# Optimization experiments

Hardware: AMD Instinct MI355X
Metric: run time of the kernel (lower is better)

Reference implementation:

```python
import jax, jax.numpy as jnp
import numpy as np

N_NODES = 4194304  # 2**22
LEVELS = 10
COARSE = 8192
RANK = 2
NNZ = 8388608


def _interp_linear(u, N):
    """torch F.interpolate(mode='linear', align_corners=False) along axis 1. u: (B,M,R) -> (B,N,R)."""
    M = u.shape[1]
    pos = (jnp.arange(N, dtype=jnp.float32) + 0.5) * (M / N) - 0.5
    pos = jnp.clip(pos, 0.0, M - 1)
    i0 = jnp.floor(pos).astype(jnp.int32)
    i1 = jnp.minimum(i0 + 1, M - 1)
    w = (pos - i0.astype(jnp.float32))[None, :, None]
    return u[:, i0] * (1.0 - w) + u[:, i1] * w


def _apply_hodlr(diag, u_factors, v_factors, x):
    B, N, _ = x.shape
    y = diag * x
    L = u_factors.shape[0]
    for lvl in range(L):
        num_splits = 2 ** (lvl + 1)
        bs = N // num_splits
        if bs == 0:
            continue
        uc, vc = u_factors[lvl], v_factors[lvl]
        u_full = _interp_linear(uc, N) if uc.shape[1] != N else uc
        v_full = _interp_linear(vc, N) if vc.shape[1] != N else vc
        P = num_splits // 2
        valid = P * 2 * bs
        xv = x[:, :valid].reshape(B, P, 2, bs, 1)
        uv = u_full[:, :valid].reshape(B, P, 2, bs, -1)
        vv = v_full[:, :valid].reshape(B, P, 2, bs, -1)
        xL, xR = xv[:, :, 0], xv[:, :, 1]
        uL, uR = uv[:, :, 0], uv[:, :, 1]
        vL, vR = vv[:, :, 0], vv[:, :, 1]
        xRp = jnp.einsum('bpkr,bpko->bpro', vR, xR)  # (B,P,R,1)
        xLp = jnp.einsum('bpkr,bpko->bpro', vL, xL)
        yL = jnp.einsum('bpkr,bpro->bpko', uL, xRp)  # (B,P,bs,1)
        yR = jnp.einsum('bpkr,bpro->bpko', uR, xLp)
        upd = jnp.stack([yL, yR], axis=2).reshape(B, valid, 1)
        if valid < N:
            upd = jnp.pad(upd, ((0, 0), (0, N - valid), (0, 0)))
        y = y + upd
    return y


def setup_inputs() -> dict:
    key = jax.random.key(0)
    ks = jax.random.split(key, 6)
    diag = jax.random.uniform(ks[0], (1, N_NODES, 1), dtype=jnp.float32)
    u_factors = jax.random.normal(ks[1], (LEVELS, 1, COARSE, RANK), dtype=jnp.float32)
    v_factors = jax.random.normal(ks[2], (LEVELS, 1, COARSE, RANK), dtype=jnp.float32)
    A_values = jax.random.normal(ks[3], (NNZ,), dtype=jnp.float32)
    z = jax.random.normal(ks[4], (1, N_NODES, 1), dtype=jnp.float32)
    A_indices = jax.random.randint(ks[5], (2, NNZ), 0, N_NODES, dtype=jnp.int64) if jax.config.jax_enable_x64 else jax.random.randint(ks[5], (2, NNZ), 0, N_NODES, dtype=jnp.int32)
    return {"diag": diag, "u_factors": u_factors, "v_factors": v_factors,
            "A_values": A_values, "z": z, "A_indices": A_indices, "num_nodes": N_NODES}


def reference(diag, u_factors, v_factors, A_values, z, A_indices, num_nodes):
    N = num_nodes
    w = _apply_hodlr(diag, u_factors, v_factors, z)          # (1,N,1)
    w_flat = w.reshape(N)
    rows, cols = A_indices[0], A_indices[1]
    y_flat = jax.ops.segment_sum(A_values * w_flat[cols], rows, num_segments=N)
    y = y_flat.reshape(1, N, 1)
    loss = jnp.mean((y - z) ** 2)
    return loss
```

## Files before the change

kernel.cpp:

```cpp
#include <hip/hip_runtime.h>

#define N_NODES 4194304
#define LEVELS  10
#define COARSE  8192
#define NNZ_E   8388608
#define NCHUNK  16384
#define NB      256
#define CB_SZ   16384
#define RB_SZ   16384
#define HB      1024
#define EPB     8192
#define TILE    8192

typedef int          v4i __attribute__((ext_vector_type(4)));
typedef float        v4f __attribute__((ext_vector_type(4)));
typedef unsigned int v4u __attribute__((ext_vector_type(4)));
typedef unsigned int v2u __attribute__((ext_vector_type(2)));

static __device__ __forceinline__ unsigned short f2bf(float x) {
    unsigned u = __float_as_uint(x);
    return (unsigned short)((u + 0x7FFFu + ((u >> 16) & 1u)) >> 16);
}
static __device__ __forceinline__ float bf2f(unsigned short h) {
    return __uint_as_float((unsigned)h << 16);
}
static __device__ __forceinline__ unsigned f18(float p) {
    return ((__float_as_uint(p) + 0x2000u) >> 14) & 0x3FFFFu;
}

__global__ __launch_bounds__(512) void kA(const float* __restrict__ z,
                                          float2* __restrict__ M,
                                          float* __restrict__ S,
                                          float* __restrict__ out,
                                          const int* __restrict__ rows,
                                          const int* __restrict__ cols,
                                          unsigned* __restrict__ colBO,
                                          unsigned* __restrict__ rowBC) {
    int b = blockIdx.x, t = threadIdx.x;
    if (b < 2048) {
        if (b == 0) {
            for (int i = t; i < 2046 * 2; i += 512) S[i] = 0.f;
            if (t == 0) out[0] = 0.f;
        }
        int lane = t & 63, wave = t >> 6;
        int chunk = b * 8 + wave;
        int base = chunk * 256 + lane * 4;
        float4 zv = *(const float4*)(z + base);
        float a0 = 0.f, a1 = 0.f;
        const float* zp = (const float*)&zv;
#pragma unroll
        for (int j = 0; j < 4; ++j) {
            float p = ((float)(base + j) + 0.5f) * (1.0f / 512.0f) - 0.5f;
            p = fminf(fmaxf(p, 0.0f), (float)(COARSE - 1));
            float f = p - floorf(p);
            a0 += zp[j] * (1.0f - f);
            a1 += zp[j] * f;
        }
#pragma unroll
        for (int off = 32; off >= 1; off >>= 1) {
            a0 += __shfl_xor(a0, off, 64);
            a1 += __shfl_xor(a1, off, 64);
        }
        if (lane == 0) M[chunk] = make_float2(a0, a1);
    } else {
        __shared__ unsigned hc[NB], hr[NB];
        int blk = b - 2048;
        if (t < 256) { hc[t] = 0u; hr[t] = 0u; }
        __syncthreads();
        int base = blk * EPB;
#pragma unroll
        for (int it = 0; it < 4; ++it) {
            int e = base + it * 2048 + t * 4;
            v4i r = __builtin_nontemporal_load((const v4i*)(rows + e));
            v4i c = __builtin_nontemporal_load((const v4i*)(cols + e));
            atomicAdd(&hr[r.x >> 14], 1u); atomicAdd(&hr[r.y >> 14], 1u);
            atomicAdd(&hr[r.z >> 14], 1u); atomicAdd(&hr[r.w >> 14], 1u);
            atomicAdd(&hc[c.x >> 14], 1u); atomicAdd(&hc[c.y >> 14], 1u);
            atomicAdd(&hc[c.z >> 14], 1u); atomicAdd(&hc[c.w >> 14], 1u);
        }
        __syncthreads();
        if (t < 256) {
            colBO[t * HB + blk] = hc[t];
            rowBC[t * HB + blk] = hr[t];
        }
    }
}

__global__ __launch_bounds__(256) void kB(const float2* __restrict__ M,
                                          const float* __restrict__ V,
                                          float* __restrict__ S,
                                          unsigned* __restrict__ colBO,
                                          unsigned* __restrict__ colTotal,
                                          const unsigned* __restrict__ rowBC,
                                          unsigned* __restrict__ rowTotal) {
    int b = blockIdx.x, t = threadIdx.x;
    if (b < 80) {
        int lvl = b >> 3, slice = b & 7;
        const float2* Vl = (const float2*)(V + lvl * COARSE * 2);
        float s0 = 0.f, s1 = 0.f;
        int c0 = slice * 2048 + t * 8;
#pragma unroll
        for (int cc = 0; cc < 8; ++cc) {
            int c = c0 + cc;
            float2 m = M[c];
            int k = (c > 0) ? ((c - 1) >> 1) : 0;
            int kp = min(k + 1, COARSE - 1);
            float2 vk = Vl[k], vkp = Vl[kp];
            s0 += vk.x * m.x + vkp.x * m.y;
            s1 += vk.y * m.x + vkp.y * m.y;
        }
        int gw = min(1 << (10 - lvl), 64);
        for (int sh = gw >> 1; sh >= 1; sh >>= 1) {
            s0 += __shfl_xor(s0, sh, 64);
            s1 += __shfl_xor(s1, sh, 64);
        }
        if ((t & (gw - 1)) == 0) {
            int bb = c0 >> (13 - lvl);
            int soff = (2 << lvl) - 2;
            unsafeAtomicAdd(&S[(soff + bb) * 2 + 0], s0);
            unsafeAtomicAdd(&S[(soff + bb) * 2 + 1], s1);
        }
    } else if (b < 336) {
        int bb = b - 80;
        __shared__ unsigned wsum[4], wbase[4];
        unsigned* p = colBO + bb * HB;
        v4u a = ((const v4u*)p)[t];
        unsigned s = a.x + a.y + a.z + a.w;
        unsigned incl = s;
#pragma unroll
        for (int off = 1; off < 64; off <<= 1) {
            unsigned n = __shfl_up(incl, off, 64);
            if ((t & 63) >= off) incl += n;
        }
        if ((t & 63) == 63) wsum[t >> 6] = incl;
        __syncthreads();
        if (t == 0) {
            unsigned acc = 0;
            for (int i = 0; i < 4; ++i) { wbase[i] = acc; acc += wsum[i]; }
            colTotal[bb] = acc;
        }
        __syncthreads();
        unsigned excl = wbase[t >> 6] + incl - s;
        v4u e;
        e.x = excl; e.y = excl + a.x; e.z = e.y + a.y; e.w = e.z + a.z;
        ((v4u*)p)[t] = e;
    } else {
        int bb = b - 336;
        __shared__ unsigned red[4];
        v4u vv = ((const v4u*)(rowBC + bb * HB))[t];
        unsigned s = vv.x + vv.y + vv.z + vv.w;
#pragma unroll
        for (int off = 32; off >= 1; off >>= 1) s += __shfl_xor(s, off, 64);
        if ((t & 63) == 0) red[t >> 6] = s;
        __syncthreads();
        if (t == 0) rowTotal[bb] = red[0] + red[1] + red[2] + red[3];
    }
}

__global__ __launch_bounds__(512) void kC(const float* __restrict__ diag,
                                          const float* __restrict__ z,
                                          const float* __restrict__ S,
                                          const float* __restrict__ U,
                                          unsigned short* __restrict__ wb,
                                          const int* __restrict__ rows,
                                          const int* __restrict__ cols,
                                          const float* __restrict__ vals,
                                          const unsigned* __restrict__ colBO,
                                          const unsigned* __restrict__ colTotal,
                                          v2u* __restrict__ colBinned,
                                          const unsigned* __restrict__ rowTotal,
                                          unsigned* __restrict__ rowCtr) {
    int b = blockIdx.x, t = threadIdx.x;
    if (b < 2048) {
        int tid = b * 512 + t;
        int base = tid * 4;
        int c = base >> 8;
        int k = (c > 0) ? ((c - 1) >> 1) : 0;
        int kp = min(k + 1, COARSE - 1);
        float g0 = 0.f, g1 = 0.f;
#pragma unroll
        for (int lvl = 0; lvl < LEVELS; ++lvl) {
            int sib = (c >> (13 - lvl)) ^ 1;
            int soff = (2 << lvl) - 2;
            float2 s2 = ((const float2*)S)[soff + sib];
            const float2* Ul = (const float2*)(U + lvl * COARSE * 2);
            float2 uk = Ul[k], ukp = Ul[kp];
            g0 += uk.x * s2.x + uk.y * s2.y;
            g1 += ukp.x * s2.x + ukp.y * s2.y;
        }
        float4 d4 = *(const float4*)(diag + base);
        float4 z4 = *(const float4*)(z + base);
        const float* dp = (const float*)&d4;
        const float* zp = (const float*)&z4;
        ushort4 h4;
        unsigned short* hp = (unsigned short*)&h4;
#pragma unroll
        for (int j = 0; j < 4; ++j) {
            float p = ((float)(base + j) + 0.5f) * (1.0f / 512.0f) - 0.5f;
            p = fminf(fmaxf(p, 0.0f), (float)(COARSE - 1));
            float f = p - floorf(p);
            hp[j] = f2bf(dp[j] * zp[j] + (g0 + f * (g1 - g0)));
        }
        *(ushort4*)(wb + base) = h4;
    } else if (b < 3072) {
        __shared__ v2u sortedP[EPB];
        __shared__ unsigned char sortedB[EPB];
        __shared__ unsigned cur[NB], gb[NB];
        __shared__ unsigned wsum[4], wbase[4];
        int blk = b - 2048;
        int base = blk * EPB;
        v4i r[4], c[4];
        v4f v[4];
#pragma unroll
        for (int j = 0; j < 4; ++j) {
            int e = base + j * 2048 + t * 4;
            r[j] = __builtin_nontemporal_load((const v4i*)(rows + e));
            c[j] = __builtin_nontemporal_load((const v4i*)(cols + e));
            v[j] = __builtin_nontemporal_load((const v4f*)(vals + e));
        }
        unsigned tv = (t < 256) ? colTotal[t] : 0u;
        unsigned incl = tv;
        if (t < 256) {
#pragma unroll
            for (int off = 1; off < 64; off <<= 1) {
                unsigned n = __shfl_up(incl, off, 64);
                if ((t & 63) >= off) incl += n;
            }
            if ((t & 63) == 63) wsum[t >> 6] = incl;
            cur[t] = 0u;
        }
        __syncthreads();
        if (t == 0) {
            unsigned a = 0;
            for (int i = 0; i < 4; ++i) { wbase[i] = a; a += wsum[i]; }
        }
        __syncthreads();
        unsigned segBase = (t < 256) ? (wbase[t >> 6] + incl - tv) : 0u;
#pragma unroll
        for (int j = 0; j < 4; ++j) {
            atomicAdd(&cur[c[j].x >> 14], 1u);
            atomicAdd(&cur[c[j].y >> 14], 1u);
            atomicAdd(&cur[c[j].z >> 14], 1u);
            atomicAdd(&cur[c[j].w >> 14], 1u);
        }
        __syncthreads();
        unsigned lv = (t < 256) ? cur[t] : 0u;
        unsigned lincl = lv;
        if (t < 256) {
#pragma unroll
            for (int off = 1; off < 64; off <<= 1) {
                unsigned n = __shfl_up(lincl, off, 64);
                if ((t & 63) >= off) lincl += n;
            }
            if ((t & 63) == 63) wsum[t >> 6] = lincl;
        }
        __syncthreads();
        if (t == 0) {
            unsigned a = 0;
            for (int i = 0; i < 4; ++i) { wbase[i] = a; a += wsum[i]; }
        }
        __syncthreads();
        if (t < 256) {
            unsigned lexcl = wbase[t >> 6] + lincl - lv;
            gb[t] = segBase + colBO[t * HB + blk] - lexcl;
            cur[t] = lexcl;
        }
        __syncthreads();
#pragma unroll
        for (int j = 0; j < 4; ++j) {
            const int* rp = (const int*)&r[j];
            const int* cp = (const int*)&c[j];
            const float* vp = (const float*)&v[j];
#pragma unroll
            for (int kk = 0; kk < 4; ++kk) {
                int row = rp[kk], col = cp[kk];
                unsigned cb = (unsigned)col >> 14;
                unsigned cl = (unsigned)col & 16383u;
                v2u ent;
                ent.x = (unsigned)row | ((cl & 0x3FFu) << 22);
                ent.y = (cl >> 10) | ((unsigned)f2bf(vp[kk]) << 16);
                unsigned i = atomicAdd(&cur[cb], 1u);
                sortedP[i] = ent;
                sortedB[i] = (unsigned char)cb;
            }
        }
        __syncthreads();
#pragma unroll
        for (int k = 0; k < 16; ++k) {
            int i = k * 512 + t;
            unsigned bkt = sortedB[i];
            __builtin_nontemporal_store(sortedP[i], colBinned + gb[bkt] + i);
        }
    } else {
        __shared__ unsigned wsum[4], wbase[4];
        unsigned tv = (t < 256) ? rowTotal[t] : 0u;
        unsigned incl = tv;
        if (t < 256) {
#pragma unroll
            for (int off = 1; off < 64; off <<= 1) {
                unsigned n = __shfl_up(incl, off, 64);
                if ((t & 63) >= off) incl += n;
            }
            if ((t & 63) == 63) wsum[t >> 6] = incl;
        }
        __syncthreads();
        if (t == 0) {
            unsigned a = 0;
            for (int i = 0; i < 4; ++i) { wbase[i] = a; a += wsum[i]; }
        }
        __syncthreads();
        if (t < 256) rowCtr[t] = wbase[t >> 6] + incl - tv;
    }
}

__global__ __launch_bounds__(512) void kD(const unsigned short* __restrict__ wb,
                                          const v2u* __restrict__ colBinned,
                                          const unsigned* __restrict__ colTotal,
                                          unsigned* __restrict__ rowCtr,
                                          unsigned* __restrict__ packed) {
    __shared__ unsigned short wSl[CB_SZ];
    __shared__ unsigned sortedP[TILE];
    __shared__ unsigned char sortedB[TILE];
    __shared__ unsigned cur[NB], gb[NB];
    __shared__ unsigned wsum[4], wbase[4];
    __shared__ unsigned sS;
    int b = blockIdx.x, t = threadIdx.x;

    unsigned tv = (t < 256) ? colTotal[t] : 0u;
    unsigned incl = tv;
    if (t < 256) {
#pragma unroll
        for (int off = 1; off < 64; off <<= 1) {
            unsigned n = __shfl_up(incl, off, 64);
            if ((t & 63) >= off) incl += n;
        }
        if ((t & 63) == 63) wsum[t >> 6] = incl;
    }
    __syncthreads();
    if (t == 0) {
        unsigned a = 0;
        for (int i = 0; i < 4; ++i) { wbase[i] = a; a += wsum[i]; }
    }
    __syncthreads();
    if (t < 256 && t == b) sS = wbase[t >> 6] + incl - tv;
    const v4u* wg = (const v4u*)(wb + (size_t)b * CB_SZ);
    for (int i = t; i < CB_SZ / 8; i += 512) ((v4u*)wSl)[i] = wg[i];
    __syncthreads();
    unsigned s0 = sS, n = colTotal[b];

    for (unsigned t0 = 0; t0 < n; t0 += TILE) {
        unsigned cnt = min((unsigned)TILE, n - t0);
        if (t < 256) cur[t] = 0u;
        __syncthreads();
        v2u ev[16];
#pragma unroll
        for (int k = 0; k < 16; ++k) {
            unsigned i = (unsigned)(k * 512 + t);
            if (i < cnt) ev[k] = __builtin_nontemporal_load(colBinned + s0 + t0 + i);
        }
#pragma unroll
        for (int k = 0; k < 16; ++k) {
            if ((unsigned)(k * 512 + t) < cnt)
                atomicAdd(&cur[(ev[k].x & 0x3FFFFFu) >> 14], 1u);
        }
        __syncthreads();
        unsigned lv = (t < 256) ? cur[t] : 0u;
        unsigned lincl = lv;
        if (t < 256) {
#pragma unroll
            for (int off = 1; off < 64; off <<= 1) {
                unsigned nn = __shfl_up(lincl, off, 64);
                if ((t & 63) >= off) lincl += nn;
            }
            if ((t & 63) == 63) wsum[t >> 6] = lincl;
        }
        __syncthreads();
        if (t == 0) {
            unsigned a = 0;
            for (int i = 0; i < 4; ++i) { wbase[i] = a; a += wsum[i]; }
        }
        __syncthreads();
        if (t < 256) {
            unsigned lexcl = wbase[t >> 6] + lincl - lv;
            gb[t] = atomicAdd(&rowCtr[t], lv) - lexcl;
            cur[t] = lexcl;
        }
        __syncthreads();
#pragma unroll
        for (int k = 0; k < 16; ++k) {
            if ((unsigned)(k * 512 + t) < cnt) {
                v2u e = ev[k];
                unsigned row = e.x & 0x3FFFFFu;
                unsigned cl = (e.x >> 22) | ((e.y & 0xFu) << 10);
                float p = bf2f((unsigned short)(e.y >> 16)) * bf2f(wSl[cl]);
                unsigned rb = row >> 14;
                unsigned i = atomicAdd(&cur[rb], 1u);
                sortedP[i] = ((row & 16383u) << 18) | f18(p);
                sortedB[i] = (unsigned char)rb;
            }
        }
        __syncthreads();
#pragma unroll
        for (int k = 0; k < 16; ++k) {
            unsigned i = (unsigned)(k * 512 + t);
            if (i < cnt) {
                unsigned bkt = sortedB[i];
                __builtin_nontemporal_store(sortedP[i], packed + gb[bkt] + i);
            }
        }
        __syncthreads();
    }
}

__global__ __launch_bounds__(1024) void kE(const unsigned* __restrict__ packed,
                                           const unsigned* __restrict__ rowTotal,
                                           const float* __restrict__ z,
                                           float* __restrict__ out) {
    __shared__ float acc[RB_SZ];
    __shared__ unsigned sb;
    __shared__ unsigned wsum[4], wbase[4];
    __shared__ float red[16];
    int b = blockIdx.x, t = threadIdx.x;

    unsigned tv = (t < 256) ? rowTotal[t] : 0u;
    unsigned incl = tv;
    if (t < 256) {
#pragma unroll
        for (int off = 1; off < 64; off <<= 1) {
            unsigned n = __shfl_up(incl, off, 64);
            if ((t & 63) >= off) incl += n;
        }
        if ((t & 63) == 63) wsum[t >> 6] = incl;
    }
    __syncthreads();
    if (t == 0) {
        unsigned a = 0;
        for (int i = 0; i < 4; ++i) { wbase[i] = a; a += wsum[i]; }
    }
    __syncthreads();
    if (t < 256 && t == b) sb = wbase[t >> 6] + incl - tv;
    for (int i = t; i < RB_SZ / 4; i += 1024) ((float4*)acc)[i] = make_float4(0.f, 0.f, 0.f, 0.f);
    __syncthreads();

    unsigned s0 = sb, n = rowTotal[b];
    for (unsigned i = t; i < n; i += 1024) {
        unsigned e = __builtin_nontemporal_load(packed + s0 + i);
        atomicAdd(&acc[e >> 18], __uint_as_float((e & 0x3FFFFu) << 14));
    }
    __syncthreads();

    float part = 0.f;
    int gbase = b * RB_SZ;
    for (int i = t; i < RB_SZ; i += 1024) {
        float d = acc[i] - z[gbase + i];
        part += d * d;
    }
#pragma unroll
    for (int off = 32; off >= 1; off >>= 1) part += __shfl_xor(part, off, 64);
    if ((t & 63) == 0) red[t >> 6] = part;
    __syncthreads();
    if (t == 0) {
        float s = 0.f;
        for (int i = 0; i < 16; ++i) s += red[i];
        unsafeAtomicAdd(out, s * (1.0f / (float)N_NODES));
    }
}

extern "C" void kernel_launch(void* const* d_in, const int* in_sizes, int n_in,
                              void* d_out, int out_size, void* d_ws, size_t ws_size,
                              hipStream_t stream) {
    const float* diag  = (const float*)d_in[0];
    const float* U     = (const float*)d_in[1];
    const float* V     = (const float*)d_in[2];
    const float* Avals = (const float*)d_in[3];
    const float* z     = (const float*)d_in[4];
    const int*   Aidx  = (const int*)d_in[5];
    const int* rows = Aidx;
    const int* cols = Aidx + NNZ_E;

    char* ws = (char*)d_ws;
    size_t off = 0;
    unsigned short* wb  = (unsigned short*)(ws + off); off += (size_t)N_NODES * 2;
    v2u* colBinned      = (v2u*)(ws + off);            off += (size_t)NNZ_E * 8;
    unsigned* packed    = (unsigned*)(ws + off);       off += (size_t)NNZ_E * 4;
    unsigned* colBO     = (unsigned*)(ws + off);       off += (size_t)NB * HB * 4;
    unsigned* rowBC     = (unsigned*)(ws + off);       off += (size_t)NB * HB * 4;
    unsigned* colTotal  = (unsigned*)(ws + off);       off += 1024;
    unsigned* rowTotal  = (unsigned*)(ws + off);       off += 1024;
    unsigned* rowCtr    = (unsigned*)(ws + off);       off += 1024;
    float2* M           = (float2*)(ws + off);         off += (size_t)NCHUNK * 8;
    float* S            = (float*)(ws + off);          off += 16384;

    kA<<<3072, 512, 0, stream>>>(z, M, S, (float*)d_out, rows, cols, colBO, rowBC);
    kB<<<592, 256, 0, stream>>>(M, V, S, colBO, colTotal, rowBC, rowTotal);
    kC<<<3073, 512, 0, stream>>>(diag, z, S, U, wb, rows, cols, Avals,
                                 colBO, colTotal, colBinned, rowTotal, rowCtr);
    kD<<<NB, 512, 0, stream>>>(wb, colBinned, colTotal, rowCtr, packed);
    kE<<<NB, 1024, 0, stream>>>(packed, rowTotal, z, (float*)d_out);
}
```

Measured before the change: 311.8 us.

## Split column bins finer and halve edges per block in binning passes

Splits the column side of the two-pass binned SpMV into 512 buckets of 8192 nodes (was 256 of 16384) and halves the edges handled per block, so twice as many histogram and scatter blocks run. The column-gather kernel now stages a smaller weight slice and gets twice as many blocks, which is meant to raise occupancy and parallelism. The bucket id is packed into spare bits of each entry, removing the separate byte array in shared memory. The cost is larger offset tables and more prefix-scan work in the bookkeeping kernel.

```diff
diff --git a/kernel.cpp b/kernel.cpp
--- a/kernel.cpp
+++ b/kernel.cpp
@@ -5,12 +5,13 @@
 #define COARSE  8192
 #define NNZ_E   8388608
 #define NCHUNK  16384
-#define NB      256
-#define CB_SZ   16384
+#define NBC     512
+#define NBR     256
+#define CB_SZ   8192
 #define RB_SZ   16384
-#define HB      1024
-#define EPB     8192
-#define TILE    8192
+#define HB      2048
+#define EPB     4096
+#define TILE    4096
 
 typedef int          v4i __attribute__((ext_vector_type(4)));
 typedef float        v4f __attribute__((ext_vector_type(4)));
@@ -63,26 +64,25 @@
         }
         if (lane == 0) M[chunk] = make_float2(a0, a1);
     } else {
-        __shared__ unsigned hc[NB], hr[NB];
+        __shared__ unsigned hc[NBC], hr[NBR];
         int blk = b - 2048;
-        if (t < 256) { hc[t] = 0u; hr[t] = 0u; }
+        for (int i = t; i < NBC; i += 512) hc[i] = 0u;
+        if (t < NBR) hr[t] = 0u;
         __syncthreads();
         int base = blk * EPB;
 #pragma unroll
-        for (int it = 0; it < 4; ++it) {
+        for (int it = 0; it < 2; ++it) {
             int e = base + it * 2048 + t * 4;
             v4i r = __builtin_nontemporal_load((const v4i*)(rows + e));
             v4i c = __builtin_nontemporal_load((const v4i*)(cols + e));
             atomicAdd(&hr[r.x >> 14], 1u); atomicAdd(&hr[r.y >> 14], 1u);
             atomicAdd(&hr[r.z >> 14], 1u); atomicAdd(&hr[r.w >> 14], 1u);
-            atomicAdd(&hc[c.x >> 14], 1u); atomicAdd(&hc[c.y >> 14], 1u);
-            atomicAdd(&hc[c.z >> 14], 1u); atomicAdd(&hc[c.w >> 14], 1u);
-        }
-        __syncthreads();
-        if (t < 256) {
-            colBO[t * HB + blk] = hc[t];
-            rowBC[t * HB + blk] = hr[t];
-        }
+            atomicAdd(&hc[c.x >> 13], 1u); atomicAdd(&hc[c.y >> 13], 1u);
+            atomicAdd(&hc[c.z >> 13], 1u); atomicAdd(&hc[c.w >> 13], 1u);
+        }
+        __syncthreads();
+        for (int i = t; i < NBC; i += 512) colBO[i * HB + blk] = hc[i];
+        if (t < NBR) rowBC[t * HB + blk] = hr[t];
     }
 }
 
@@ -120,12 +120,13 @@
             unsafeAtomicAdd(&S[(soff + bb) * 2 + 0], s0);
             unsafeAtomicAdd(&S[(soff + bb) * 2 + 1], s1);
         }
-    } else if (b < 336) {
+    } else if (b < 592) {
         int bb = b - 80;
         __shared__ unsigned wsum[4], wbase[4];
         unsigned* p = colBO + bb * HB;
-        v4u a = ((const v4u*)p)[t];
-        unsigned s = a.x + a.y + a.z + a.w;
+        v4u a = *(const v4u*)(p + t * 8);
+        v4u c = *(const v4u*)(p + t * 8 + 4);
+        unsigned s = a.x + a.y + a.z + a.w + c.x + c.y + c.z + c.w;
         unsigned incl = s;
 #pragma unroll
         for (int off = 1; off < 64; off <<= 1) {
@@ -141,14 +142,17 @@
         }
         __syncthreads();
         unsigned excl = wbase[t >> 6] + incl - s;
-        v4u e;
-        e.x = excl; e.y = excl + a.x; e.z = e.y + a.y; e.w = e.z + a.z;
-        ((v4u*)p)[t] = e;
+        v4u e0, e1;
+        e0.x = excl;       e0.y = e0.x + a.x; e0.z = e0.y + a.y; e0.w = e0.z + a.z;
+        e1.x = e0.w + a.w; e1.y = e1.x + c.x; e1.z = e1.y + c.y; e1.w = e1.z + c.z;
+        *(v4u*)(p + t * 8) = e0;
+        *(v4u*)(p + t * 8 + 4) = e1;
     } else {
-        int bb = b - 336;
+        int bb = b - 592;
         __shared__ unsigned red[4];
-        v4u vv = ((const v4u*)(rowBC + bb * HB))[t];
-        unsigned s = vv.x + vv.y + vv.z + vv.w;
+        v4u a = *(const v4u*)(rowBC + bb * HB + t * 8);
+        v4u c = *(const v4u*)(rowBC + bb * HB + t * 8 + 4);
+        unsigned s = a.x + a.y + a.z + a.w + c.x + c.y + c.z + c.w;
 #pragma unroll
         for (int off = 32; off >= 1; off >>= 1) s += __shfl_xor(s, off, 64);
         if ((t & 63) == 0) red[t >> 6] = s;
@@ -202,94 +206,88 @@
             hp[j] = f2bf(dp[j] * zp[j] + (g0 + f * (g1 - g0)));
         }
         *(ushort4*)(wb + base) = h4;
-    } else if (b < 3072) {
+    } else if (b < 4096) {
         __shared__ v2u sortedP[EPB];
-        __shared__ unsigned char sortedB[EPB];
-        __shared__ unsigned cur[NB], gb[NB];
-        __shared__ unsigned wsum[4], wbase[4];
+        __shared__ unsigned cur[NBC], gb[NBC];
+        __shared__ unsigned wsum[8], wbase[8];
         int blk = b - 2048;
         int base = blk * EPB;
-        v4i r[4], c[4];
-        v4f v[4];
-#pragma unroll
-        for (int j = 0; j < 4; ++j) {
+        v4i r[2], c[2];
+        v4f v[2];
+#pragma unroll
+        for (int j = 0; j < 2; ++j) {
             int e = base + j * 2048 + t * 4;
             r[j] = __builtin_nontemporal_load((const v4i*)(rows + e));
             c[j] = __builtin_nontemporal_load((const v4i*)(cols + e));
             v[j] = __builtin_nontemporal_load((const v4f*)(vals + e));
         }
-        unsigned tv = (t < 256) ? colTotal[t] : 0u;
+        unsigned tv = colTotal[t];
         unsigned incl = tv;
-        if (t < 256) {
-#pragma unroll
-            for (int off = 1; off < 64; off <<= 1) {
-                unsigned n = __shfl_up(incl, off, 64);
-                if ((t & 63) >= off) incl += n;
-            }
-            if ((t & 63) == 63) wsum[t >> 6] = incl;
-            cur[t] = 0u;
-        }
+#pragma unroll
+        for (int off = 1; off < 64; off <<= 1) {
+            unsigned n = __shfl_up(incl, off, 64);
+            if ((t & 63) >= off) incl += n;
+        }
+        if ((t & 63) == 63) wsum[t >> 6] = incl;
+        cur[t] = 0u;
         __syncthreads();
         if (t == 0) {
             unsigned a = 0;
-            for (int i = 0; i < 4; ++i) { wbase[i] = a; a += wsum[i]; }
-        }
-        __syncthreads();
-        unsigned segBase = (t < 256) ? (wbase[t >> 6] + incl - tv) : 0u;
-#pragma unroll
-        for (int j = 0; j < 4; ++j) {
-            atomicAdd(&cur[c[j].x >> 14], 1u);
-            atomicAdd(&cur[c[j].y >> 14], 1u);
-            atomicAdd(&cur[c[j].z >> 14], 1u);
-            atomicAdd(&cur[c[j].w >> 14], 1u);
-        }
-        __syncthreads();
-        unsigned lv = (t < 256) ? cur[t] : 0u;
+            for (int i = 0; i < 8; ++i) { wbase[i] = a; a += wsum[i]; }
+        }
+        __syncthreads();
+        unsigned segBase = wbase[t >> 6] + incl - tv;
+#pragma unroll
+        for (int j = 0; j < 2; ++j) {
+            atomicAdd(&cur[c[j].x >> 13], 1u);
+            atomicAdd(&cur[c[j].y >> 13], 1u);
+            atomicAdd(&cur[c[j].z >> 13], 1u);
+            atomicAdd(&cur[c[j].w >> 13], 1u);
+        }
+        __syncthreads();
+        unsigned lv = cur[t];
         unsigned lincl = lv;
-        if (t < 256) {
-#pragma unroll
-            for (int off = 1; off < 64; off <<= 1) {
-                unsigned n = __shfl_up(lincl, off, 64);
-                if ((t & 63) >= off) lincl += n;
-            }
-            if ((t & 63) == 63) wsum[t >> 6] = lincl;
-        }
+#pragma unroll
+        for (int off = 1; off < 64; off <<= 1) {
+            unsigned n = __shfl_up(lincl, off, 64);
+            if ((t & 63) >= off) lincl += n;
+        }
+        if ((t & 63) == 63) wsum[t >> 6] = lincl;
         __syncthreads();
         if (t == 0) {
             unsigned a = 0;
-            for (int i = 0; i < 4; ++i) { wbase[i] = a; a += wsum[i]; }
-        }
-        __syncthreads();
-        if (t < 256) {
-            unsigned lexcl = wbase[t >> 6] + lincl - lv;
-            gb[t] = segBase + colBO[t * HB + blk] - lexcl;
-            cur[t] = lexcl;
-        }
-        __syncthreads();
-#pragma unroll
-        for (int j = 0; j < 4; ++j) {
+            for (int i = 0; i < 8; ++i) { wbase[i] = a; a += wsum[i]; }
+        }
+        __syncthreads();
+        unsigned lexcl = wbase[t >> 6] + lincl - lv;
+        gb[t] = segBase + colBO[t * HB + blk] - lexcl;
+        __syncthreads();
+        cur[t] = lexcl;
+        __syncthreads();
+#pragma unroll
+        for (int j = 0; j < 2; ++j) {
             const int* rp = (const int*)&r[j];
             const int* cp = (const int*)&c[j];
             const float* vp = (const float*)&v[j];
 #pragma unroll
             for (int kk = 0; kk < 4; ++kk) {
                 int row = rp[kk], col = cp[kk];
-                unsigned cb = (unsigned)col >> 14;
-                unsigned cl = (unsigned)col & 16383u;
+                unsigned cb = (unsigned)col >> 13;
+                unsigned cl = (unsigned)col & 8191u;
                 v2u ent;
                 ent.x = (unsigned)row | ((cl & 0x3FFu) << 22);
-                ent.y = (cl >> 10) | ((unsigned)f2bf(vp[kk]) << 16);
+                ent.y = (cl >> 10) | (cb << 3) | ((unsigned)f2bf(vp[kk]) << 16);
                 unsigned i = atomicAdd(&cur[cb], 1u);
                 sortedP[i] = ent;
-                sortedB[i] = (unsigned char)cb;
             }
         }
         __syncthreads();
 #pragma unroll
-        for (int k = 0; k < 16; ++k) {
+        for (int k = 0; k < 8; ++k) {
             int i = k * 512 + t;
-            unsigned bkt = sortedB[i];
-            __builtin_nontemporal_store(sortedP[i], colBinned + gb[bkt] + i);
+            v2u ent = sortedP[i];
+            unsigned bkt = (ent.y >> 3) & 0x1FFu;
+            __builtin_nontemporal_store(ent, colBinned + gb[bkt] + i);
         }
     } else {
         __shared__ unsigned wsum[4], wbase[4];
@@ -321,28 +319,26 @@
     __shared__ unsigned short wSl[CB_SZ];
     __shared__ unsigned sortedP[TILE];
     __shared__ unsigned char sortedB[TILE];
-    __shared__ unsigned cur[NB], gb[NB];
-    __shared__ unsigned wsum[4], wbase[4];
+    __shared__ unsigned cur[NBR], gb[NBR];
+    __shared__ unsigned wsum[8], wbase[8];
     __shared__ unsigned sS;
     int b = blockIdx.x, t = threadIdx.x;
 
-    unsigned tv = (t < 256) ? colTotal[t] : 0u;
+    unsigned tv = colTotal[t];
     unsigned incl = tv;
-    if (t < 256) {
-#pragma unroll
-        for (int off = 1; off < 64; off <<= 1) {
-            unsigned n = __shfl_up(incl, off, 64);
-            if ((t & 63) >= off) incl += n;
-        }
-        if ((t & 63) == 63) wsum[t >> 6] = incl;
-    }
+#pragma unroll
+    for (int off = 1; off < 64; off <<= 1) {
+        unsigned n = __shfl_up(incl, off, 64);
+        if ((t & 63) >= off) incl += n;
+    }
+    if ((t & 63) == 63) wsum[t >> 6] = incl;
     __syncthreads();
     if (t == 0) {
         unsigned a = 0;
-        for (int i = 0; i < 4; ++i) { wbase[i] = a; a += wsum[i]; }
-    }
-    __syncthreads();
-    if (t < 256 && t == b) sS = wbase[t >> 6] + incl - tv;
+        for (int i = 0; i < 8; ++i) { wbase[i] = a; a += wsum[i]; }
+    }
+    __syncthreads();
+    if (t == b) sS = wbase[t >> 6] + incl - tv;
     const v4u* wg = (const v4u*)(wb + (size_t)b * CB_SZ);
     for (int i = t; i < CB_SZ / 8; i += 512) ((v4u*)wSl)[i] = wg[i];
     __syncthreads();
@@ -350,23 +346,23 @@
 
     for (unsigned t0 = 0; t0 < n; t0 += TILE) {
         unsigned cnt = min((unsigned)TILE, n - t0);
-        if (t < 256) cur[t] = 0u;
-        __syncthreads();
-        v2u ev[16];
-#pragma unroll
-        for (int k = 0; k < 16; ++k) {
+        if (t < NBR) cur[t] = 0u;
+        __syncthreads();
+        v2u ev[8];
+#pragma unroll
+        for (int k = 0; k < 8; ++k) {
             unsigned i = (unsigned)(k * 512 + t);
             if (i < cnt) ev[k] = __builtin_nontemporal_load(colBinned + s0 + t0 + i);
         }
 #pragma unroll
-        for (int k = 0; k < 16; ++k) {
+        for (int k = 0; k < 8; ++k) {
             if ((unsigned)(k * 512 + t) < cnt)
                 atomicAdd(&cur[(ev[k].x & 0x3FFFFFu) >> 14], 1u);
         }
         __syncthreads();
-        unsigned lv = (t < 256) ? cur[t] : 0u;
+        unsigned lv = (t < NBR) ? cur[t] : 0u;
         unsigned lincl = lv;
-        if (t < 256) {
+        if (t < NBR) {
 #pragma unroll
             for (int off = 1; off < 64; off <<= 1) {
                 unsigned nn = __shfl_up(lincl, off, 64);
@@ -380,18 +376,18 @@
             for (int i = 0; i < 4; ++i) { wbase[i] = a; a += wsum[i]; }
         }
         __syncthreads();
-        if (t < 256) {
+        if (t < NBR) {
             unsigned lexcl = wbase[t >> 6] + lincl - lv;
             gb[t] = atomicAdd(&rowCtr[t], lv) - lexcl;
             cur[t] = lexcl;
         }
         __syncthreads();
 #pragma unroll
-        for (int k = 0; k < 16; ++k) {
+        for (int k = 0; k < 8; ++k) {
             if ((unsigned)(k * 512 + t) < cnt) {
                 v2u e = ev[k];
                 unsigned row = e.x & 0x3FFFFFu;
-                unsigned cl = (e.x >> 22) | ((e.y & 0xFu) << 10);
+                unsigned cl = (e.x >> 22) | ((e.y & 0x7u) << 10);
                 float p = bf2f((unsigned short)(e.y >> 16)) * bf2f(wSl[cl]);
                 unsigned rb = row >> 14;
                 unsigned i = atomicAdd(&cur[rb], 1u);
@@ -401,7 +397,7 @@
         }
         __syncthreads();
 #pragma unroll
-        for (int k = 0; k < 16; ++k) {
+        for (int k = 0; k < 8; ++k) {
             unsigned i = (unsigned)(k * 512 + t);
             if (i < cnt) {
                 unsigned bkt = sortedB[i];
@@ -483,18 +479,18 @@
     unsigned short* wb  = (unsigned short*)(ws + off); off += (size_t)N_NODES * 2;
     v2u* colBinned      = (v2u*)(ws + off);            off += (size_t)NNZ_E * 8;
     unsigned* packed    = (unsigned*)(ws + off);       off += (size_t)NNZ_E * 4;
-    unsigned* colBO     = (unsigned*)(ws + off);       off += (size_t)NB * HB * 4;
-    unsigned* rowBC     = (unsigned*)(ws + off);       off += (size_t)NB * HB * 4;
-    unsigned* colTotal  = (unsigned*)(ws + off);       off += 1024;
-    unsigned* rowTotal  = (unsigned*)(ws + off);       off += 1024;
-    unsigned* rowCtr    = (unsigned*)(ws + off);       off += 1024;
+    unsigned* colBO     = (unsigned*)(ws + off);       off += (size_t)NBC * HB * 4;
+    unsigned* rowBC     = (unsigned*)(ws + off);       off += (size_t)NBR * HB * 4;
+    unsigned* colTotal  = (unsigned*)(ws + off);       off += NBC * 4;
+    unsigned* rowTotal  = (unsigned*)(ws + off);       off += NBR * 4;
+    unsigned* rowCtr    = (unsigned*)(ws + off);       off += NBR * 4;
     float2* M           = (float2*)(ws + off);         off += (size_t)NCHUNK * 8;
     float* S            = (float*)(ws + off);          off += 16384;
 
-    kA<<<3072, 512, 0, stream>>>(z, M, S, (float*)d_out, rows, cols, colBO, rowBC);
-    kB<<<592, 256, 0, stream>>>(M, V, S, colBO, colTotal, rowBC, rowTotal);
-    kC<<<3073, 512, 0, stream>>>(diag, z, S, U, wb, rows, cols, Avals,
+    kA<<<4096, 512, 0, stream>>>(z, M, S, (float*)d_out, rows, cols, colBO, rowBC);
+    kB<<<848, 256, 0, stream>>>(M, V, S, colBO, colTotal, rowBC, rowTotal);
+    kC<<<4097, 512, 0, stream>>>(diag, z, S, U, wb, rows, cols, Avals,
                                  colBO, colTotal, colBinned, rowTotal, rowCtr);
-    kD<<<NB, 512, 0, stream>>>(wb, colBinned, colTotal, rowCtr, packed);
-    kE<<<NB, 1024, 0, stream>>>(packed, rowTotal, z, (float*)d_out);
-}
+    kD<<<NBC, 512, 0, stream>>>(wb, colBinned, colTotal, rowCtr, packed);
+    kE<<<NBR, 1024, 0, stream>>>(packed, rowTotal, z, (float*)d_out);
+}
```

Result: slower. 366.0 us (+17.4%).
